# Kernel tuning notes

Measured on AMD Instinct MI355X. Metric: run time of the kernel, lower is better.

Reference implementation:

```python
import jax, jax.numpy as jnp
import numpy as np
import math

B, S, D, H, L, W, DFF = 2, 4096, 768, 12, 4, 128, 3072
DH = D // H  # head dim = 64
EPS = 1e-6


def layer_norm(x, g, b):
    mu = jnp.mean(x, axis=-1, keepdims=True)
    var = jnp.mean(jnp.square(x - mu), axis=-1, keepdims=True)
    return (x - mu) * jax.lax.rsqrt(var + EPS) * g + b


def band_attn(x, Wq, bq, Wk, bk, Wv, bv):
    """Longformer sliding_chunks attention, window W on each side. x: (B,S,D)."""
    q = (x @ Wq + bq).reshape(B, S, H, DH).transpose(0, 2, 1, 3) / math.sqrt(DH)
    k = (x @ Wk + bk).reshape(B, S, H, DH).transpose(0, 2, 1, 3)
    v = (x @ Wv + bv).reshape(B, S, H, DH).transpose(0, 2, 1, 3)
    nc = S // W  # number of query chunks of size W
    # pad keys/values with W zeros each side; masked out below
    kp = jnp.pad(k, ((0, 0), (0, 0), (W, W), (0, 0)))
    vp = jnp.pad(v, ((0, 0), (0, 0), (W, W), (0, 0)))
    kb = kp.reshape(B, H, nc + 2, W, DH)
    vb = vp.reshape(B, H, nc + 2, W, DH)
    # key chunk for query chunk c covers global keys [c*W - W, c*W + 2W)
    kc = jnp.concatenate([kb[:, :, :-2], kb[:, :, 1:-1], kb[:, :, 2:]], axis=3)  # (B,H,nc,3W,DH)
    vc = jnp.concatenate([vb[:, :, :-2], vb[:, :, 1:-1], vb[:, :, 2:]], axis=3)
    qc = q.reshape(B, H, nc, W, DH)
    scores = jnp.einsum('bhcqd,bhckd->bhcqk', qc, kc)  # (B,H,nc,W,3W)
    # valid iff |j-i| <= W and 0 <= j < S, where i = c*W+qi, j = c*W+ki-W
    qi = jnp.arange(W)[:, None]
    ki = jnp.arange(3 * W)[None, :]
    band = jnp.abs(ki - W - qi) <= W  # (W,3W)
    c = jnp.arange(nc)[:, None, None]
    j = c * W + ki[None] - W  # (nc,1,3W) broadcast
    valid = band[None] & (j >= 0) & (j < S)  # (nc,W,3W)
    neg = jnp.finfo(scores.dtype).min
    scores = jnp.where(valid[None, None], scores, neg)
    probs = jax.nn.softmax(scores, axis=-1)
    out = jnp.einsum('bhcqk,bhckd->bhcqd', probs, vc)  # (B,H,nc,W,DH)
    return out.reshape(B, H, S, DH).transpose(0, 2, 1, 3).reshape(B, S, D)


def setup_inputs() -> dict:
    key = jax.random.key(0)
    ks = jax.random.split(key, 8)
    init = lambda k, shape: (jax.random.normal(k, shape) * 0.02).astype(jnp.float32)
    return {
        'src': jax.random.normal(ks[0], (B, S, D), dtype=jnp.float32),
        'Wq': init(ks[1], (L, D, D)), 'bq': jnp.zeros((L, D), jnp.float32),
        'Wk': init(ks[2], (L, D, D)), 'bk': jnp.zeros((L, D), jnp.float32),
        'Wv': init(ks[3], (L, D, D)), 'bv': jnp.zeros((L, D), jnp.float32),
        'W1': init(ks[4], (L, D, DFF)), 'b1': jnp.zeros((L, DFF), jnp.float32),
        'W2': init(ks[5], (L, DFF, D)), 'b2': jnp.zeros((L, D), jnp.float32),
        'ln2_g': jnp.ones((L, D), jnp.float32), 'ln2_b': jnp.zeros((L, D), jnp.float32),
        'lnf_g': jnp.ones((D,), jnp.float32), 'lnf_b': jnp.zeros((D,), jnp.float32),
    }


def reference(src, Wq, bq, Wk, bk, Wv, bv, W1, b1, W2, b2, ln2_g, ln2_b, lnf_g, lnf_b):
    x = src
    for i in range(L):
        # post-norm layer: note norm1 is dead code in the original when normalize_before=False
        x = x + band_attn(x, Wq[i], bq[i], Wk[i], bk[i], Wv[i], bv[i])
        h = jnp.maximum(x @ W1[i] + b1[i], 0.0) @ W2[i] + b2[i]
        x = layer_norm(x + h, ln2_g[i], ln2_b[i])
    return layer_norm(x, lnf_g, lnf_b)
```

## Files before the change

### kernel.cpp

```cpp
#include <hip/hip_runtime.h>

typedef __bf16 bf16;
typedef __bf16 bf16x8 __attribute__((ext_vector_type(8)));
typedef float floatx4 __attribute__((ext_vector_type(4)));

#define MFMA16(a, b, c) __builtin_amdgcn_mfma_f32_16x16x32_bf16((a), (b), (c), 0, 0, 0)
#define NEG_SENT -30000.0f

#define GLOAD_LDS16(gp, lp)                                                              \
    __builtin_amdgcn_global_load_lds((const __attribute__((address_space(1))) void*)(gp), \
                                     (__attribute__((address_space(3))) void*)(lp), 16, 0, 0)


__device__ __forceinline__ float ldin(const void* p, size_t i, int isb)
{
    return isb ? (float)((const bf16*)p)[i] : ((const float*)p)[i];
}

__global__ __launch_bounds__(256) void sniff_kernel(const unsigned short* __restrict__ s,
                                                    int* __restrict__ flag)
{
    __shared__ int cnt;
    if (threadIdx.x == 0) cnt = 0;
    __syncthreads();
    int good = 0;
    #pragma unroll
    for (int t = 0; t < 16; ++t) {
        unsigned short h = s[threadIdx.x * 16 + t];
        int e = (h >> 7) & 0xFF;
        if (h == 0 || (e >= 96 && e <= 158)) good++;
    }
    atomicAdd(&cnt, good);
    __syncthreads();
    if (threadIdx.x == 0) *flag = (cnt >= 3700) ? 1 : 0;
}

__global__ __launch_bounds__(256) void cvt_src_kernel(const void* __restrict__ s,
                                                      float* __restrict__ x,
                                                      bf16* __restrict__ xb, int n,
                                                      const int* __restrict__ flag)
{
    const int isb = *flag;
    const int stride = gridDim.x * 256;
    if (xb) {
        for (int i = blockIdx.x * 256 + threadIdx.x; i < n; i += stride) {
            float v = ldin(s, i, isb);
            x[i] = v; xb[i] = (bf16)v;
        }
    } else {
        for (int i = blockIdx.x * 256 + threadIdx.x; i < n; i += stride)
            x[i] = ldin(s, i, isb);
    }
}

__global__ __launch_bounds__(256) void prep_kernel(
    const void* __restrict__ bq, const void* __restrict__ bk, const void* __restrict__ bv,
    const void* __restrict__ b1, const void* __restrict__ b2,
    const void* __restrict__ ln2g, const void* __restrict__ ln2b,
    const void* __restrict__ lnfg, const void* __restrict__ lnfb,
    float* __restrict__ dst, const int* __restrict__ flag)
{
    const int isb = *flag;
    int i = blockIdx.x * 256 + threadIdx.x;
    if (i < 9216) {
        int l = i / 2304, c = i % 2304;
        float v = (c < 768)  ? ldin(bq, l * 768 + c, isb)
                : (c < 1536) ? ldin(bk, l * 768 + c - 768, isb)
                             : ldin(bv, l * 768 + c - 1536, isb);
        dst[i] = v; return;
    }
    i -= 9216;
    if (i < 12288) { dst[9216 + i]  = ldin(b1, i, isb);   return; } i -= 12288;
    if (i < 3072)  { dst[21504 + i] = ldin(b2, i, isb);   return; } i -= 3072;
    if (i < 3072)  { dst[24576 + i] = ldin(ln2g, i, isb); return; } i -= 3072;
    if (i < 3072)  { dst[27648 + i] = ldin(ln2b, i, isb); return; } i -= 3072;
    if (i < 768)   { dst[30720 + i] = ldin(lnfg, i, isb); return; } i -= 768;
    if (i < 768)   { dst[31488 + i] = ldin(lnfb, i, isb); return; }
}

__global__ __launch_bounds__(256) void transpose_kernel(const void* __restrict__ src,
                                                        size_t eoff, bf16* __restrict__ dst,
                                                        int K, int N,
                                                        const int* __restrict__ flag)
{
    __shared__ bf16 tile[64][65];
    const int isb = *flag;
    const int n0 = blockIdx.x * 64, k0 = blockIdx.y * 64;
    const int tid = threadIdx.x;
    #pragma unroll
    for (int it = 0; it < 16; ++it) {
        int idx = it * 256 + tid;
        int r = idx >> 6, c = idx & 63;
        tile[r][c] = (bf16)ldin(src, eoff + (size_t)(k0 + r) * N + (n0 + c), isb);
    }
    __syncthreads();
    #pragma unroll
    for (int it = 0; it < 16; ++it) {
        int idx = it * 256 + tid;
        int r = idx >> 6, c = idx & 63;
        dst[(size_t)(n0 + r) * K + (k0 + c)] = tile[c][r];
    }
}

__global__ __launch_bounds__(256) void transpose3_kernel(const void* __restrict__ Wq,
                                                         const void* __restrict__ Wk,
                                                         const void* __restrict__ Wv,
                                                         size_t eoff, bf16* __restrict__ dst,
                                                         const int* __restrict__ flag)
{
    __shared__ bf16 tile[64][65];
    const int isb = *flag;
    const void* src = (blockIdx.z == 0) ? Wq : (blockIdx.z == 1) ? Wk : Wv;
    bf16* d = dst + (size_t)blockIdx.z * 768 * 768;
    const int n0 = blockIdx.x * 64, k0 = blockIdx.y * 64;
    const int tid = threadIdx.x;
    #pragma unroll
    for (int it = 0; it < 16; ++it) {
        int idx = it * 256 + tid;
        int r = idx >> 6, c = idx & 63;
        tile[r][c] = (bf16)ldin(src, eoff + (size_t)(k0 + r) * 768 + (n0 + c), isb);
    }
    __syncthreads();
    #pragma unroll
    for (int it = 0; it < 16; ++it) {
        int idx = it * 256 + tid;
        int r = idx >> 6, c = idx & 63;
        d[(size_t)(n0 + r) * 768 + (k0 + c)] = tile[c][r];
    }
}

template<int AM>
__global__ __launch_bounds__(256, 4) void gemm_kernel(
    const void* __restrict__ A, int a_f32, const bf16* __restrict__ Bt,
    const float* __restrict__ bias,
    bf16* __restrict__ outb, float* __restrict__ outf,
    int M, int N, int K, int mode, int scale_cols)
{
    constexpr int BM = AM * 32;
    constexpr int BN = 128;
    __shared__ __align__(16) bf16 smem[(BM + BN) * 64];
    bf16* As = smem;
    bf16* Bs = smem + BM * 64;

    const int tid = threadIdx.x;
    const int m0 = blockIdx.y * BM, n0 = blockIdx.x * BN;
    const int lane = tid & 63, wave = tid >> 6;
    const int wr = (wave >> 1) * (AM * 16), wc = (wave & 1) * 64;
    const int l16 = lane & 15, quad = lane >> 4;
    const int lrow = lane >> 3, lcol = (lane & 7) * 8;

    floatx4 acc[AM][4];
    #pragma unroll
    for (int i = 0; i < AM; ++i)
        #pragma unroll
        for (int j = 0; j < 4; ++j)
            #pragma unroll
            for (int r = 0; r < 4; ++r) acc[i][j][r] = 0.f;

    for (int k0 = 0; k0 < K; k0 += 64) {
        if (a_f32) {
            const float* Af = (const float*)A;
            #pragma unroll
            for (int it = 0; it < AM; ++it) {
                int chunk = it * 256 + tid;
                int row = chunk >> 3, c8 = (chunk & 7) * 8;
                size_t off = (size_t)(m0 + row) * K + k0 + c8;
                float4 f0 = *(const float4*)&Af[off];
                float4 f1 = *(const float4*)&Af[off + 4];
                bf16x8 v;
                v[0] = (bf16)f0.x; v[1] = (bf16)f0.y; v[2] = (bf16)f0.z; v[3] = (bf16)f0.w;
                v[4] = (bf16)f1.x; v[5] = (bf16)f1.y; v[6] = (bf16)f1.z; v[7] = (bf16)f1.w;
                *(bf16x8*)&As[row * 64 + c8] = v;
            }
            for (int s = wave; s < BN / 8; s += 4) {
                const bf16* gp = Bt + (size_t)(n0 + s * 8 + lrow) * K + k0 + lcol;
                GLOAD_LDS16(gp, Bs + s * 512);
            }
        } else {
            const bf16* Ab = (const bf16*)A;
            for (int s = wave; s < (BM + BN) / 8; s += 4) {
                const bf16* gp; bf16* lp;
                if (s < BM / 8) {
                    gp = Ab + (size_t)(m0 + s * 8 + lrow) * K + k0 + lcol;
                    lp = As + s * 512;
                } else {
                    int s2 = s - BM / 8;
                    gp = Bt + (size_t)(n0 + s2 * 8 + lrow) * K + k0 + lcol;
                    lp = Bs + s2 * 512;
                }
                GLOAD_LDS16(gp, lp);
            }
        }
        __syncthreads();
        #pragma unroll
        for (int kk = 0; kk < 64; kk += 32) {
            bf16x8 af[AM], bv[4];
            #pragma unroll
            for (int i = 0; i < AM; ++i) af[i] = *(const bf16x8*)&As[(wr + i * 16 + l16) * 64 + kk + quad * 8];
            #pragma unroll
            for (int j = 0; j < 4; ++j)  bv[j] = *(const bf16x8*)&Bs[(wc + j * 16 + l16) * 64 + kk + quad * 8];
            #pragma unroll
            for (int i = 0; i < AM; ++i)
                #pragma unroll
                for (int j = 0; j < 4; ++j)
                    acc[i][j] = MFMA16(af[i], bv[j], acc[i][j]);
        }
        __syncthreads();
    }

    #pragma unroll
    for (int j = 0; j < 4; ++j) {
        int col = n0 + wc + j * 16 + l16;
        float bs = bias[col];
        float alpha = (col < scale_cols) ? 0.125f : 1.0f;
        #pragma unroll
        for (int i = 0; i < AM; ++i) {
            #pragma unroll
            for (int r = 0; r < 4; ++r) {
                int row = m0 + wr + i * 16 + quad * 4 + r;
                size_t idx = (size_t)row * N + col;
                float v = (acc[i][j][r] + bs) * alpha;
                if (mode == 0)      outb[idx] = (bf16)v;
                else if (mode == 1) outb[idx] = (bf16)fmaxf(v, 0.f);
                else                outf[idx] += v;
            }
        }
    }
}

__global__ __launch_bounds__(256, 2) void attn_kernel(const bf16* __restrict__ qkv,
                                                      float* __restrict__ x,
                                                      bf16* __restrict__ xb)
{
    __shared__ __align__(16) bf16 Ks[128 * 64];
    __shared__ __align__(16) bf16 Vt[64 * 136];
    __shared__ __align__(16) bf16 Ps[128 * 136];

    const int c = blockIdx.x, h = blockIdx.y, b = blockIdx.z;
    const int tid = threadIdx.x;
    const int lane = tid & 63, w = tid >> 6;
    const int l16 = lane & 15, quad = lane >> 4;
    const int lrow = lane >> 3, lcol = (lane & 7) * 8;
    const size_t rowbase = (size_t)(b * 4096 + c * 128);

    bf16x8 aq[2][2];
    #pragma unroll
    for (int i = 0; i < 2; ++i)
        #pragma unroll
        for (int kh = 0; kh < 2; ++kh)
            aq[i][kh] = *(const bf16x8*)&qkv[(rowbase + w * 32 + i * 16 + l16) * 2304 + h * 64 + kh * 32 + quad * 8];

    floatx4 o[2][4], mr[2], lr[2];
    #pragma unroll
    for (int i = 0; i < 2; ++i) {
        #pragma unroll
        for (int r = 0; r < 4; ++r) { mr[i][r] = NEG_SENT; lr[i][r] = 0.f; }
        #pragma unroll
        for (int tv = 0; tv < 4; ++tv)
            #pragma unroll
            for (int r = 0; r < 4; ++r) o[i][tv][r] = 0.f;
    }

    const int t0 = (c == 0) ? 1 : 0;
    const int t1 = (c == 31) ? 1 : 2;
    for (int t = t0; t <= t1; ++t) {
        const size_t kb = (size_t)(b * 4096 + c * 128 + (t - 1) * 128);
        __syncthreads();
        for (int s = w; s < 16; s += 4) {
            const bf16* gp = &qkv[(kb + s * 8 + lrow) * 2304 + 768 + h * 64 + lcol];
            GLOAD_LDS16(gp, Ks + s * 512);
        }
        for (int idx = tid; idx < 8192; idx += 256) {
            int key = idx >> 6, dh = idx & 63;
            Vt[dh * 136 + key] = qkv[(kb + key) * 2304 + 1536 + h * 64 + dh];
        }
        __syncthreads();

        floatx4 st[2][8];
        #pragma unroll
        for (int i = 0; i < 2; ++i)
            #pragma unroll
            for (int j = 0; j < 8; ++j)
                #pragma unroll
                for (int r = 0; r < 4; ++r) st[i][j][r] = 0.f;
        #pragma unroll
        for (int kh = 0; kh < 2; ++kh) {
            #pragma unroll
            for (int j = 0; j < 8; ++j) {
                bf16x8 bk = *(const bf16x8*)&Ks[(j * 16 + l16) * 64 + kh * 32 + quad * 8];
                st[0][j] = MFMA16(aq[0][kh], bk, st[0][j]);
                st[1][j] = MFMA16(aq[1][kh], bk, st[1][j]);
            }
        }
        if (t != 1) {
            #pragma unroll
            for (int i = 0; i < 2; ++i)
                #pragma unroll
                for (int j = 0; j < 8; ++j)
                    #pragma unroll
                    for (int r = 0; r < 4; ++r) {
                        int qi = w * 32 + i * 16 + quad * 4 + r;
                        int ki = j * 16 + l16;
                        bool valid = (t == 0) ? (ki >= qi) : (ki <= qi);
                        if (!valid) st[i][j][r] = NEG_SENT;
                    }
        }
        #pragma unroll
        for (int i = 0; i < 2; ++i) {
            floatx4 mx = st[i][0];
            #pragma unroll
            for (int j = 1; j < 8; ++j)
                #pragma unroll
                for (int r = 0; r < 4; ++r) mx[r] = fmaxf(mx[r], st[i][j][r]);
            #pragma unroll
            for (int r = 0; r < 4; ++r) {
                float v = mx[r];
                #pragma unroll
                for (int off = 1; off < 16; off <<= 1) v = fmaxf(v, __shfl_xor(v, off, 64));
                mx[r] = v;
            }
            floatx4 scale;
            #pragma unroll
            for (int r = 0; r < 4; ++r) {
                float mnew = fmaxf(mr[i][r], mx[r]);
                scale[r] = __expf(mr[i][r] - mnew);
                mr[i][r] = mnew;
            }
            floatx4 psum;
            #pragma unroll
            for (int r = 0; r < 4; ++r) psum[r] = 0.f;
            #pragma unroll
            for (int j = 0; j < 8; ++j)
                #pragma unroll
                for (int r = 0; r < 4; ++r) {
                    float p = __expf(st[i][j][r] - mr[i][r]);
                    psum[r] += p;
                    Ps[(w * 32 + i * 16 + quad * 4 + r) * 136 + j * 16 + l16] = (bf16)p;
                }
            #pragma unroll
            for (int r = 0; r < 4; ++r) {
                float v = psum[r];
                #pragma unroll
                for (int off = 1; off < 16; off <<= 1) v += __shfl_xor(v, off, 64);
                lr[i][r] = lr[i][r] * scale[r] + v;
            }
            #pragma unroll
            for (int tv = 0; tv < 4; ++tv)
                #pragma unroll
                for (int r = 0; r < 4; ++r) o[i][tv][r] *= scale[r];
        }
        __syncthreads();
        #pragma unroll
        for (int kk = 0; kk < 128; kk += 32) {
            bf16x8 ap0 = *(const bf16x8*)&Ps[(w * 32 + l16) * 136 + kk + quad * 8];
            bf16x8 ap1 = *(const bf16x8*)&Ps[(w * 32 + 16 + l16) * 136 + kk + quad * 8];
            #pragma unroll
            for (int tv = 0; tv < 4; ++tv) {
                bf16x8 bv = *(const bf16x8*)&Vt[(tv * 16 + l16) * 136 + kk + quad * 8];
                o[0][tv] = MFMA16(ap0, bv, o[0][tv]);
                o[1][tv] = MFMA16(ap1, bv, o[1][tv]);
            }
        }
    }

    #pragma unroll
    for (int i = 0; i < 2; ++i)
        #pragma unroll
        for (int r = 0; r < 4; ++r) {
            int srow = w * 32 + i * 16 + quad * 4 + r;
            size_t base = (rowbase + srow) * 768 + h * 64;
            float inv = 1.f / lr[i][r];
            #pragma unroll
            for (int tv = 0; tv < 4; ++tv) {
                size_t idx = base + tv * 16 + l16;
                float val = x[idx] + o[i][tv][r] * inv;
                x[idx] = val;
                if (xb) xb[idx] = (bf16)val;
            }
        }
}

__global__ __launch_bounds__(256) void ln_kernel(const float* in,
                                                 const float* __restrict__ g,
                                                 const float* __restrict__ be,
                                                 float* out, bf16* outb)
{
    const int wv = threadIdx.x >> 6, lane = threadIdx.x & 63;
    const size_t row = (size_t)blockIdx.x * 4 + wv;
    const float* r = in + row * 768;
    float v[12], s = 0.f, sq = 0.f;
    #pragma unroll
    for (int j = 0; j < 12; ++j) {
        float t = r[j * 64 + lane];
        v[j] = t; s += t; sq += t * t;
    }
    #pragma unroll
    for (int off = 1; off < 64; off <<= 1) {
        s += __shfl_xor(s, off, 64);
        sq += __shfl_xor(sq, off, 64);
    }
    const float mu = s * (1.f / 768.f);
    const float var = sq * (1.f / 768.f) - mu * mu;
    const float rs = rsqrtf(var + 1e-6f);
    #pragma unroll
    for (int j = 0; j < 12; ++j) {
        int col = j * 64 + lane;
        float y = (v[j] - mu) * rs * g[col] + be[col];
        out[row * 768 + col] = y;
        if (outb) outb[row * 768 + col] = (bf16)y;
    }
}

__global__ __launch_bounds__(256) void ln_final_kernel(const float* __restrict__ in,
                                                       const float* __restrict__ g,
                                                       const float* __restrict__ be,
                                                       void* __restrict__ out,
                                                       const int* __restrict__ flag)
{
    const int isb = *flag;
    const int wv = threadIdx.x >> 6, lane = threadIdx.x & 63;
    const size_t row = (size_t)blockIdx.x * 4 + wv;
    const float* r = in + row * 768;
    float v[12], s = 0.f, sq = 0.f;
    #pragma unroll
    for (int j = 0; j < 12; ++j) {
        float t = r[j * 64 + lane];
        v[j] = t; s += t; sq += t * t;
    }
    #pragma unroll
    for (int off = 1; off < 64; off <<= 1) {
        s += __shfl_xor(s, off, 64);
        sq += __shfl_xor(sq, off, 64);
    }
    const float mu = s * (1.f / 768.f);
    const float var = sq * (1.f / 768.f) - mu * mu;
    const float rs = rsqrtf(var + 1e-6f);
    #pragma unroll
    for (int j = 0; j < 12; ++j) {
        int col = j * 64 + lane;
        float y = (v[j] - mu) * rs * g[col] + be[col];
        if (isb) ((bf16*)out)[row * 768 + col] = (bf16)y;
        else     ((float*)out)[row * 768 + col] = y;
    }
}

extern "C" void kernel_launch(void* const* d_in, const int* in_sizes, int n_in,
                              void* d_out, int out_size, void* d_ws, size_t ws_size,
                              hipStream_t stream)
{
    const void* src  = d_in[0];
    const void* Wq   = d_in[1];
    const void* bq   = d_in[2];
    const void* Wk   = d_in[3];
    const void* bk   = d_in[4];
    const void* Wv   = d_in[5];
    const void* bv   = d_in[6];
    const void* W1   = d_in[7];
    const void* b1   = d_in[8];
    const void* W2   = d_in[9];
    const void* b2   = d_in[10];
    const void* ln2g = d_in[11];
    const void* ln2b = d_in[12];
    const void* lnfg = d_in[13];
    const void* lnfb = d_in[14];

    const size_t SZ_X   = 8192ull * 768 * 4;
    const size_t SZ_XB  = 8192ull * 768 * 2;
    const size_t SZ_QKV = 8192ull * 2304 * 2;
    const size_t SZ_H1F = 8192ull * 3072 * 2;
    const size_t SZ_W1  = 3072ull * 768 * 2;
    const size_t SZ_W2  = 4718592;
    const size_t SMALL  = 131072;
    const size_t needA = SZ_X + SZ_XB + SZ_H1F + SZ_W1 + SZ_W2 + SMALL;
    const size_t needB = SZ_X + SZ_XB + SZ_QKV + SZ_W1 + SZ_W2 + SMALL;
    const int lay = (ws_size >= needA) ? 2 : (ws_size >= needB) ? 1 : 0;

    char* p = (char*)d_ws;
    float* x = (float*)p;  p += SZ_X;
    bf16* xb = nullptr;
    if (lay) { xb = (bf16*)p; p += SZ_XB; }
    bf16* sh  = (bf16*)p;  p += (lay == 2) ? SZ_H1F : SZ_QKV;
    bf16* wT  = (bf16*)p;  p += SZ_W1;
    bf16* w2T = (bf16*)p;  p += SZ_W2;
    float* sm = (float*)p;
    float* qbias = sm;          float* b1c = sm + 9216;   float* b2c = sm + 21504;
    float* ln2gc = sm + 24576;  float* ln2bc = sm + 27648;
    float* lnfgc = sm + 30720;  float* lnfbc = sm + 31488;
    int* flag = (int*)(sm + 32256);

    sniff_kernel<<<1, 256, 0, stream>>>((const unsigned short*)src, flag);
    cvt_src_kernel<<<1024, 256, 0, stream>>>(src, x, xb, 8192 * 768, flag);
    prep_kernel<<<126, 256, 0, stream>>>(bq, bk, bv, b1, b2, ln2g, ln2b, lnfg, lnfb, sm, flag);

    for (int i = 0; i < 4; ++i) {
        const size_t woQ = (size_t)i * 768 * 768;
        const size_t wo1 = (size_t)i * 768 * 3072;
        const size_t wo2 = (size_t)i * 3072 * 768;

        transpose3_kernel<<<dim3(12, 12, 3), 256, 0, stream>>>(Wq, Wk, Wv, woQ, wT, flag);

        if (lay)
            gemm_kernel<4><<<dim3(18, 64), 256, 0, stream>>>(xb, 0, wT, qbias + i * 2304,
                                                             sh, nullptr, 8192, 2304, 768, 0, 768);
        else
            gemm_kernel<4><<<dim3(18, 64), 256, 0, stream>>>(x, 1, wT, qbias + i * 2304,
                                                             sh, nullptr, 8192, 2304, 768, 0, 768);
        attn_kernel<<<dim3(32, 12, 2), 256, 0, stream>>>(sh, x, xb);

        transpose_kernel<<<dim3(48, 12), 256, 0, stream>>>(W1, wo1, wT, 768, 3072, flag);
        transpose_kernel<<<dim3(12, 48), 256, 0, stream>>>(W2, wo2, w2T, 3072, 768, flag);

        if (lay == 2) {
            gemm_kernel<4><<<dim3(24, 64), 256, 0, stream>>>(xb, 0, wT, b1c + i * 3072,
                                                             sh, nullptr, 8192, 3072, 768, 1, 0);
            gemm_kernel<2><<<dim3(6, 128), 256, 0, stream>>>(sh, 0, w2T, b2c + i * 768,
                                                             nullptr, x, 8192, 768, 3072, 2, 0);
        } else {
            for (int half = 0; half < 2; ++half) {
                float* xh = x + (size_t)half * 4096 * 768;
                const void* A1 = lay ? (const void*)(xb + (size_t)half * 4096 * 768) : (const void*)xh;
                gemm_kernel<4><<<dim3(24, 32), 256, 0, stream>>>(A1, lay ? 0 : 1, wT, b1c + i * 3072,
                                                                 sh, nullptr, 4096, 3072, 768, 1, 0);
                gemm_kernel<2><<<dim3(6, 64), 256, 0, stream>>>(sh, 0, w2T, b2c + i * 768,
                                                                nullptr, xh, 4096, 768, 3072, 2, 0);
            }
        }
        ln_kernel<<<2048, 256, 0, stream>>>(x, ln2gc + i * 768, ln2bc + i * 768, x, xb);
    }
    ln_final_kernel<<<2048, 256, 0, stream>>>(x, lnfgc, lnfbc, d_out, flag);
}
```

Baseline: 1.488 ms.

## Split-K FFN2 GEMM with atomics, merge W1/W2 transposes, restructure attention PV

```diff
diff --git a/kernel.cpp b/kernel.cpp
--- a/kernel.cpp
+++ b/kernel.cpp
@@ -11,6 +11,8 @@
     __builtin_amdgcn_global_load_lds((const __attribute__((address_space(1))) void*)(gp), \
                                      (__attribute__((address_space(3))) void*)(lp), 16, 0, 0)
 
+
+__device__ __forceinline__ void atomAddF(float* p, float v) { unsafeAtomicAdd(p, v); }
 
 __device__ __forceinline__ float ldin(const void* p, size_t i, int isb)
 {
@@ -78,30 +80,6 @@
     if (i < 768)   { dst[31488 + i] = ldin(lnfb, i, isb); return; }
 }
 
-__global__ __launch_bounds__(256) void transpose_kernel(const void* __restrict__ src,
-                                                        size_t eoff, bf16* __restrict__ dst,
-                                                        int K, int N,
-                                                        const int* __restrict__ flag)
-{
-    __shared__ bf16 tile[64][65];
-    const int isb = *flag;
-    const int n0 = blockIdx.x * 64, k0 = blockIdx.y * 64;
-    const int tid = threadIdx.x;
-    #pragma unroll
-    for (int it = 0; it < 16; ++it) {
-        int idx = it * 256 + tid;
-        int r = idx >> 6, c = idx & 63;
-        tile[r][c] = (bf16)ldin(src, eoff + (size_t)(k0 + r) * N + (n0 + c), isb);
-    }
-    __syncthreads();
-    #pragma unroll
-    for (int it = 0; it < 16; ++it) {
-        int idx = it * 256 + tid;
-        int r = idx >> 6, c = idx & 63;
-        dst[(size_t)(n0 + r) * K + (k0 + c)] = tile[c][r];
-    }
-}
-
 __global__ __launch_bounds__(256) void transpose3_kernel(const void* __restrict__ Wq,
                                                          const void* __restrict__ Wk,
                                                          const void* __restrict__ Wv,
@@ -129,11 +107,41 @@
     }
 }
 
+__global__ __launch_bounds__(256) void transpose12_kernel(const void* __restrict__ W1,
+                                                          size_t eoff1, bf16* __restrict__ d1,
+                                                          const void* __restrict__ W2,
+                                                          size_t eoff2, bf16* __restrict__ d2,
+                                                          const int* __restrict__ flag)
+{
+    __shared__ bf16 tile[64][65];
+    const int isb = *flag;
+    const int z = blockIdx.z;
+    const void* src = z ? W2 : W1;
+    const size_t eoff = z ? eoff2 : eoff1;
+    bf16* d = z ? d2 : d1;
+    const int K = z ? 3072 : 768, N = z ? 768 : 3072;
+    const int n0 = (z ? blockIdx.y : blockIdx.x) * 64;
+    const int k0 = (z ? blockIdx.x : blockIdx.y) * 64;
+    const int tid = threadIdx.x;
+    #pragma unroll
+    for (int it = 0; it < 16; ++it) {
+        int idx = it * 256 + tid;
+        int r = idx >> 6, c = idx & 63;
+        tile[r][c] = (bf16)ldin(src, eoff + (size_t)(k0 + r) * N + (n0 + c), isb);
+    }
+    __syncthreads();
+    #pragma unroll
+    for (int it = 0; it < 16; ++it) {
+        int idx = it * 256 + tid;
+        int r = idx >> 6, c = idx & 63;
+        d[(size_t)(n0 + r) * K + (k0 + c)] = tile[c][r];
+    }
+}
+
 template<int AM>
 __global__ __launch_bounds__(256, 4) void gemm_kernel(
     const void* __restrict__ A, int a_f32, const bf16* __restrict__ Bt,
-    const float* __restrict__ bias,
-    bf16* __restrict__ outb, float* __restrict__ outf,
+    const float* __restrict__ bias, bf16* __restrict__ outb,
     int M, int N, int K, int mode, int scale_cols)
 {
     constexpr int BM = AM * 32;
@@ -220,21 +228,94 @@
                 int row = m0 + wr + i * 16 + quad * 4 + r;
                 size_t idx = (size_t)row * N + col;
                 float v = (acc[i][j][r] + bs) * alpha;
-                if (mode == 0)      outb[idx] = (bf16)v;
-                else if (mode == 1) outb[idx] = (bf16)fmaxf(v, 0.f);
-                else                outf[idx] += v;
-            }
-        }
-    }
-}
-
-__global__ __launch_bounds__(256, 2) void attn_kernel(const bf16* __restrict__ qkv,
+                if (mode == 0) outb[idx] = (bf16)v;
+                else           outb[idx] = (bf16)fmaxf(v, 0.f);
+            }
+        }
+    }
+}
+
+__global__ __launch_bounds__(256, 4) void gemm_sk_kernel(
+    const bf16* __restrict__ A, const bf16* __restrict__ Bt,
+    const float* __restrict__ bias, float* __restrict__ outf,
+    int M, int N, int K)
+{
+    constexpr int BM = 128, BN = 128;
+    __shared__ __align__(16) bf16 smem[(BM + BN) * 64];
+    bf16* As = smem;
+    bf16* Bs = smem + BM * 64;
+
+    const int tid = threadIdx.x;
+    const int m0 = blockIdx.y * BM, n0 = blockIdx.x * BN;
+    const int kbeg = blockIdx.z * (K >> 1), kend = kbeg + (K >> 1);
+    const int lane = tid & 63, wave = tid >> 6;
+    const int wr = (wave >> 1) * 64, wc = (wave & 1) * 64;
+    const int l16 = lane & 15, quad = lane >> 4;
+    const int lrow = lane >> 3, lcol = (lane & 7) * 8;
+
+    floatx4 acc[4][4];
+    #pragma unroll
+    for (int i = 0; i < 4; ++i)
+        #pragma unroll
+        for (int j = 0; j < 4; ++j)
+            #pragma unroll
+            for (int r = 0; r < 4; ++r) acc[i][j][r] = 0.f;
+
+    for (int k0 = kbeg; k0 < kend; k0 += 64) {
+        for (int s = wave; s < 32; s += 4) {
+            const bf16* gp; bf16* lp;
+            if (s < 16) {
+                gp = A + (size_t)(m0 + s * 8 + lrow) * K + k0 + lcol;
+                lp = As + s * 512;
+            } else {
+                int s2 = s - 16;
+                gp = Bt + (size_t)(n0 + s2 * 8 + lrow) * K + k0 + lcol;
+                lp = Bs + s2 * 512;
+            }
+            GLOAD_LDS16(gp, lp);
+        }
+        __syncthreads();
+        #pragma unroll
+        for (int kk = 0; kk < 64; kk += 32) {
+            bf16x8 af[4], bv[4];
+            #pragma unroll
+            for (int i = 0; i < 4; ++i) af[i] = *(const bf16x8*)&As[(wr + i * 16 + l16) * 64 + kk + quad * 8];
+            #pragma unroll
+            for (int j = 0; j < 4; ++j) bv[j] = *(const bf16x8*)&Bs[(wc + j * 16 + l16) * 64 + kk + quad * 8];
+            #pragma unroll
+            for (int i = 0; i < 4; ++i)
+                #pragma unroll
+                for (int j = 0; j < 4; ++j)
+                    acc[i][j] = MFMA16(af[i], bv[j], acc[i][j]);
+        }
+        __syncthreads();
+    }
+
+    const float bscale = (blockIdx.z == 0) ? 1.f : 0.f;
+    #pragma unroll
+    for (int j = 0; j < 4; ++j) {
+        int col = n0 + wc + j * 16 + l16;
+        float bs = bias[col] * bscale;
+        #pragma unroll
+        for (int i = 0; i < 4; ++i) {
+            #pragma unroll
+            for (int r = 0; r < 4; ++r) {
+                int row = m0 + wr + i * 16 + quad * 4 + r;
+                atomAddF(&outf[(size_t)row * N + col], acc[i][j][r] + bs);
+            }
+        }
+    }
+}
+
+#define VOFF(d) ((d) * 136 + ((d) >> 3) * 8)
+#define POFF(q) ((q) * 72 + ((q) >> 3) * 8)
+__global__ __launch_bounds__(256, 3) void attn_kernel(const bf16* __restrict__ qkv,
                                                       float* __restrict__ x,
                                                       bf16* __restrict__ xb)
 {
     __shared__ __align__(16) bf16 Ks[128 * 64];
-    __shared__ __align__(16) bf16 Vt[64 * 136];
-    __shared__ __align__(16) bf16 Ps[128 * 136];
+    __shared__ __align__(16) bf16 Vt[64 * 136 + 64];
+    __shared__ __align__(16) bf16 Ps[128 * 72 + 128];
 
     const int c = blockIdx.x, h = blockIdx.y, b = blockIdx.z;
     const int tid = threadIdx.x;
@@ -270,9 +351,13 @@
             const bf16* gp = &qkv[(kb + s * 8 + lrow) * 2304 + 768 + h * 64 + lcol];
             GLOAD_LDS16(gp, Ks + s * 512);
         }
-        for (int idx = tid; idx < 8192; idx += 256) {
-            int key = idx >> 6, dh = idx & 63;
-            Vt[dh * 136 + key] = qkv[(kb + key) * 2304 + 1536 + h * 64 + dh];
+        #pragma unroll
+        for (int it = 0; it < 4; ++it) {
+            int tsk = it * 256 + tid;
+            int cc = tsk & 7, key = tsk >> 3;
+            bf16x8 v = *(const bf16x8*)&qkv[(kb + key) * 2304 + 1536 + h * 64 + cc * 8];
+            #pragma unroll
+            for (int j = 0; j < 8; ++j) Vt[VOFF(cc * 8 + j) + key] = v[j];
         }
         __syncthreads();
 
@@ -305,6 +390,7 @@
                         if (!valid) st[i][j][r] = NEG_SENT;
                     }
         }
+        floatx4 scale[2], psum[2];
         #pragma unroll
         for (int i = 0; i < 2; ++i) {
             floatx4 mx = st[i][0];
@@ -317,50 +403,49 @@
                 float v = mx[r];
                 #pragma unroll
                 for (int off = 1; off < 16; off <<= 1) v = fmaxf(v, __shfl_xor(v, off, 64));
-                mx[r] = v;
-            }
-            floatx4 scale;
+                float mnew = fmaxf(mr[i][r], v);
+                scale[i][r] = __expf(mr[i][r] - mnew);
+                mr[i][r] = mnew;
+                psum[i][r] = 0.f;
+            }
+            #pragma unroll
+            for (int tv = 0; tv < 4; ++tv)
+                #pragma unroll
+                for (int r = 0; r < 4; ++r) o[i][tv][r] *= scale[i][r];
+        }
+        #pragma unroll
+        for (int ph = 0; ph < 2; ++ph) {
+            #pragma unroll
+            for (int i = 0; i < 2; ++i)
+                #pragma unroll
+                for (int j4 = 0; j4 < 4; ++j4)
+                    #pragma unroll
+                    for (int r = 0; r < 4; ++r) {
+                        float p = __expf(st[i][ph * 4 + j4][r] - mr[i][r]);
+                        psum[i][r] += p;
+                        Ps[POFF(w * 32 + i * 16 + quad * 4 + r) + j4 * 16 + l16] = (bf16)p;
+                    }
+            #pragma unroll
+            for (int kk2 = 0; kk2 < 64; kk2 += 32) {
+                bf16x8 ap0 = *(const bf16x8*)&Ps[POFF(w * 32 + l16) + kk2 + quad * 8];
+                bf16x8 ap1 = *(const bf16x8*)&Ps[POFF(w * 32 + 16 + l16) + kk2 + quad * 8];
+                #pragma unroll
+                for (int tv = 0; tv < 4; ++tv) {
+                    bf16x8 bv = *(const bf16x8*)&Vt[VOFF(tv * 16 + l16) + ph * 64 + kk2 + quad * 8];
+                    o[0][tv] = MFMA16(ap0, bv, o[0][tv]);
+                    o[1][tv] = MFMA16(ap1, bv, o[1][tv]);
+                }
+            }
+        }
+        #pragma unroll
+        for (int i = 0; i < 2; ++i)
             #pragma unroll
             for (int r = 0; r < 4; ++r) {
-                float mnew = fmaxf(mr[i][r], mx[r]);
-                scale[r] = __expf(mr[i][r] - mnew);
-                mr[i][r] = mnew;
-            }
-            floatx4 psum;
-            #pragma unroll
-            for (int r = 0; r < 4; ++r) psum[r] = 0.f;
-            #pragma unroll
-            for (int j = 0; j < 8; ++j)
-                #pragma unroll
-                for (int r = 0; r < 4; ++r) {
-                    float p = __expf(st[i][j][r] - mr[i][r]);
-                    psum[r] += p;
-                    Ps[(w * 32 + i * 16 + quad * 4 + r) * 136 + j * 16 + l16] = (bf16)p;
-                }
-            #pragma unroll
-            for (int r = 0; r < 4; ++r) {
-                float v = psum[r];
+                float v = psum[i][r];
                 #pragma unroll
                 for (int off = 1; off < 16; off <<= 1) v += __shfl_xor(v, off, 64);
-                lr[i][r] = lr[i][r] * scale[r] + v;
-            }
-            #pragma unroll
-            for (int tv = 0; tv < 4; ++tv)
-                #pragma unroll
-                for (int r = 0; r < 4; ++r) o[i][tv][r] *= scale[r];
-        }
-        __syncthreads();
-        #pragma unroll
-        for (int kk = 0; kk < 128; kk += 32) {
-            bf16x8 ap0 = *(const bf16x8*)&Ps[(w * 32 + l16) * 136 + kk + quad * 8];
-            bf16x8 ap1 = *(const bf16x8*)&Ps[(w * 32 + 16 + l16) * 136 + kk + quad * 8];
-            #pragma unroll
-            for (int tv = 0; tv < 4; ++tv) {
-                bf16x8 bv = *(const bf16x8*)&Vt[(tv * 16 + l16) * 136 + kk + quad * 8];
-                o[0][tv] = MFMA16(ap0, bv, o[0][tv]);
-                o[1][tv] = MFMA16(ap1, bv, o[1][tv]);
-            }
-        }
+                lr[i][r] = lr[i][r] * scale[i][r] + v;
+            }
     }
 
     #pragma unroll
@@ -501,28 +586,27 @@
 
         if (lay)
             gemm_kernel<4><<<dim3(18, 64), 256, 0, stream>>>(xb, 0, wT, qbias + i * 2304,
-                                                             sh, nullptr, 8192, 2304, 768, 0, 768);
+                                                             sh, 8192, 2304, 768, 0, 768);
         else
             gemm_kernel<4><<<dim3(18, 64), 256, 0, stream>>>(x, 1, wT, qbias + i * 2304,
-                                                             sh, nullptr, 8192, 2304, 768, 0, 768);
+                                                             sh, 8192, 2304, 768, 0, 768);
         attn_kernel<<<dim3(32, 12, 2), 256, 0, stream>>>(sh, x, xb);
 
-        transpose_kernel<<<dim3(48, 12), 256, 0, stream>>>(W1, wo1, wT, 768, 3072, flag);
-        transpose_kernel<<<dim3(12, 48), 256, 0, stream>>>(W2, wo2, w2T, 3072, 768, flag);
+        transpose12_kernel<<<dim3(48, 12, 2), 256, 0, stream>>>(W1, wo1, wT, W2, wo2, w2T, flag);
 
         if (lay == 2) {
             gemm_kernel<4><<<dim3(24, 64), 256, 0, stream>>>(xb, 0, wT, b1c + i * 3072,
-                                                             sh, nullptr, 8192, 3072, 768, 1, 0);
-            gemm_kernel<2><<<dim3(6, 128), 256, 0, stream>>>(sh, 0, w2T, b2c + i * 768,
-                                                             nullptr, x, 8192, 768, 3072, 2, 0);
+                                                             sh, 8192, 3072, 768, 1, 0);
+            gemm_sk_kernel<<<dim3(6, 64, 2), 256, 0, stream>>>(sh, w2T, b2c + i * 768,
+                                                               x, 8192, 768, 3072);
         } else {
             for (int half = 0; half < 2; ++half) {
                 float* xh = x + (size_t)half * 4096 * 768;
                 const void* A1 = lay ? (const void*)(xb + (size_t)half * 4096 * 768) : (const void*)xh;
                 gemm_kernel<4><<<dim3(24, 32), 256, 0, stream>>>(A1, lay ? 0 : 1, wT, b1c + i * 3072,
-                                                                 sh, nullptr, 4096, 3072, 768, 1, 0);
-                gemm_kernel<2><<<dim3(6, 64), 256, 0, stream>>>(sh, 0, w2T, b2c + i * 768,
-                                                                nullptr, xh, 4096, 768, 3072, 2, 0);
+                                                                 sh, 4096, 3072, 768, 1, 0);
+                gemm_sk_kernel<<<dim3(6, 32, 2), 256, 0, stream>>>(sh, w2T, b2c + i * 768,
+                                                                   xh, 4096, 768, 3072);
             }
         }
         ln_kernel<<<2048, 256, 0, stream>>>(x, ln2gc + i * 768, ln2bc + i * 768, x, xb);
```

Result: faster. 1.387 ms (-6.8%).
